# Kernel optimization log

Hardware: AMD Instinct MI355X
Metric: run time of the kernel (lower is better)

Reference implementation:

```python
import jax, jax.numpy as jnp
import numpy as np

V = 50257       # vocab size (leaves of Huffman tree)
N_DEC = V - 1   # internal decision nodes
D = 1024        # input_size
N_EX = 8192     # number of examples (tokens)
MAX_LEN = 24    # max Huffman path depth


def setup_inputs() -> dict:
    key = jax.random.key(0)
    k_x, k_w, k_t, k_p, k_c, k_l = jax.random.split(key, 6)
    x = jax.random.normal(k_x, (N_EX, D), dtype=jnp.float32)
    W = jax.random.normal(k_w, (N_DEC, D), dtype=jnp.float32) * 0.02
    t = jax.random.randint(k_t, (N_EX,), 0, V, dtype=jnp.int32)
    # padded per-leaf tree paths: decision-node indices and +/-1 branch codes
    paths = jax.random.randint(k_p, (V, MAX_LEN), 0, N_DEC, dtype=jnp.int32)
    codes = jnp.where(jax.random.bernoulli(k_c, 0.5, (V, MAX_LEN)), 1.0, -1.0).astype(jnp.float32)
    lens = jax.random.randint(k_l, (V,), 1, MAX_LEN + 1, dtype=jnp.int32)
    return {"x": x, "W": W, "t": t, "paths": paths, "codes": codes, "lens": lens}


def reference(x, W, t, paths, codes, lens):
    # Per-example tree path: gather the decision nodes / codes for each target leaf.
    node_idx = paths[t]            # [N_EX, MAX_LEN] int32
    code = codes[t]                # [N_EX, MAX_LEN] +/-1
    mask = (jnp.arange(MAX_LEN)[None, :] < lens[t][:, None]).astype(x.dtype)  # [N_EX, MAX_LEN]
    # Irregular gather of W rows along each path, then per-step dot products.
    Wp = W[node_idx]               # [N_EX, MAX_LEN, D]
    wxy = code * jnp.einsum('nd,nld->nl', x, Wp)   # [N_EX, MAX_LEN]
    # Per-decision binary log-loss: log(1 + exp(-wxy)), masked to true path length.
    ls = jax.nn.softplus(-wxy) * mask
    return ls.sum()
```

## Files before the change

### kernel.cpp

```cpp
#include <hip/hip_runtime.h>
#include <math.h>

#define HS_D       1024
#define HS_MAXLEN  24
#define HS_SPW     6

__global__ __launch_bounds__(256) void hsm_loss_kernel(
    const float* __restrict__ x,
    const float* __restrict__ W,
    const int*   __restrict__ t,
    const int*   __restrict__ paths,
    const float* __restrict__ codes,
    const int*   __restrict__ lens,
    float*       __restrict__ out)
{
    const int n    = blockIdx.x;
    const int tid  = threadIdx.x;
    const int wave = tid >> 6;
    const int lane = tid & 63;

    const int leaf = t[n];
    const int L    = lens[leaf];

    int   node[HS_SPW];
    float code[HS_SPW];
#pragma unroll
    for (int s = 0; s < HS_SPW; ++s) {
        const int l = wave + 4 * s;
        node[s] = paths[leaf * HS_MAXLEN + l];
        code[s] = codes[leaf * HS_MAXLEN + l];
    }

    const float4* x4 = (const float4*)(x + (size_t)n * HS_D);
    float4 xf[4];
#pragma unroll
    for (int j = 0; j < 4; ++j)
        xf[j] = x4[j * 64 + lane];

    float4 wf[HS_SPW][4];
#pragma unroll
    for (int s = 0; s < HS_SPW; ++s) {
        const float4* w4 = (const float4*)(W + (size_t)node[s] * HS_D);
#pragma unroll
        for (int j = 0; j < 4; ++j)
            wf[s][j] = w4[j * 64 + lane];
    }

    float dot[HS_SPW];
#pragma unroll
    for (int s = 0; s < HS_SPW; ++s) {
        float d = 0.0f;
#pragma unroll
        for (int j = 0; j < 4; ++j) {
            d += xf[j].x * wf[s][j].x + xf[j].y * wf[s][j].y
               + xf[j].z * wf[s][j].z + xf[j].w * wf[s][j].w;
        }
        dot[s] = d;
    }

#pragma unroll
    for (int off = 32; off > 0; off >>= 1) {
#pragma unroll
        for (int s = 0; s < HS_SPW; ++s)
            dot[s] += __shfl_down(dot[s], off);
    }

    float local = 0.0f;
    if (lane == 0) {
#pragma unroll
        for (int s = 0; s < HS_SPW; ++s) {
            const int l = wave + 4 * s;
            const float z = -code[s] * dot[s];
            const float sp = fmaxf(z, 0.0f) + log1pf(expf(-fabsf(z)));
            local += (l < L) ? sp : 0.0f;
        }
    }

    __shared__ float sred[4];
    if (lane == 0) sred[wave] = local;
    __syncthreads();
    if (tid == 0) {
        const float blocksum = sred[0] + sred[1] + sred[2] + sred[3];
        atomicAdd(out, blocksum);
    }
}

extern "C" void kernel_launch(void* const* d_in, const int* in_sizes, int n_in,
                              void* d_out, int out_size, void* d_ws, size_t ws_size,
                              hipStream_t stream) {
    const float* x     = (const float*)d_in[0];
    const float* W     = (const float*)d_in[1];
    const int*   t     = (const int*)  d_in[2];
    const int*   paths = (const int*)  d_in[3];
    const float* codes = (const float*)d_in[4];
    const int*   lens  = (const int*)  d_in[5];
    float* out = (float*)d_out;

    const int n_ex = in_sizes[2];

    hipMemsetAsync(out, 0, sizeof(float), stream);

    hsm_loss_kernel<<<n_ex, 256, 0, stream>>>(x, W, t, paths, codes, lens, out);
}
```

Before: 394.0 us.

## Assign one example per wave, loop only over valid path steps, bucket atomics

Each wavefront now handles a single example, broadcasts that example's path nodes and codes with lane shuffles, and walks only the first L steps in groups of four. Before, every step up to the maximum depth was loaded whether or not it was masked out. This removes the W row gathers for padded steps, which are on average about half of all steps. The single global atomic is replaced by atomics spread over 512 workspace buckets, summed by a small second kernel. The trade-offs are wave divergence from uneven path lengths, an extra kernel launch plus a larger memset, and possibly less memory-level parallelism per wave.

```diff
diff --git a/kernel.cpp b/kernel.cpp
--- a/kernel.cpp
+++ b/kernel.cpp
@@ -3,33 +3,23 @@
 
 #define HS_D       1024
 #define HS_MAXLEN  24
-#define HS_SPW     6
+#define HS_NBUCKET 512
 
-__global__ __launch_bounds__(256) void hsm_loss_kernel(
+__global__ __launch_bounds__(256, 4) void hsm_wave_kernel(
     const float* __restrict__ x,
     const float* __restrict__ W,
     const int*   __restrict__ t,
     const int*   __restrict__ paths,
     const float* __restrict__ codes,
     const int*   __restrict__ lens,
-    float*       __restrict__ out)
+    float*       __restrict__ ws)
 {
-    const int n    = blockIdx.x;
     const int tid  = threadIdx.x;
-    const int wave = tid >> 6;
     const int lane = tid & 63;
+    const int n    = blockIdx.x * 4 + (tid >> 6);
 
     const int leaf = t[n];
     const int L    = lens[leaf];
-
-    int   node[HS_SPW];
-    float code[HS_SPW];
-#pragma unroll
-    for (int s = 0; s < HS_SPW; ++s) {
-        const int l = wave + 4 * s;
-        node[s] = paths[leaf * HS_MAXLEN + l];
-        code[s] = codes[leaf * HS_MAXLEN + l];
-    }
 
     const float4* x4 = (const float4*)(x + (size_t)n * HS_D);
     float4 xf[4];
@@ -37,52 +27,80 @@
     for (int j = 0; j < 4; ++j)
         xf[j] = x4[j * 64 + lane];
 
-    float4 wf[HS_SPW][4];
-#pragma unroll
-    for (int s = 0; s < HS_SPW; ++s) {
-        const float4* w4 = (const float4*)(W + (size_t)node[s] * HS_D);
-#pragma unroll
-        for (int j = 0; j < 4; ++j)
-            wf[s][j] = w4[j * 64 + lane];
-    }
-
-    float dot[HS_SPW];
-#pragma unroll
-    for (int s = 0; s < HS_SPW; ++s) {
-        float d = 0.0f;
-#pragma unroll
-        for (int j = 0; j < 4; ++j) {
-            d += xf[j].x * wf[s][j].x + xf[j].y * wf[s][j].y
-               + xf[j].z * wf[s][j].z + xf[j].w * wf[s][j].w;
-        }
-        dot[s] = d;
-    }
-
-#pragma unroll
-    for (int off = 32; off > 0; off >>= 1) {
-#pragma unroll
-        for (int s = 0; s < HS_SPW; ++s)
-            dot[s] += __shfl_down(dot[s], off);
+    int   node_l = 0;
+    float code_l = 0.0f;
+    if (lane < HS_MAXLEN) {
+        node_l = paths[leaf * HS_MAXLEN + lane];
+        code_l = codes[leaf * HS_MAXLEN + lane];
     }
 
     float local = 0.0f;
-    if (lane == 0) {
+
+    for (int b = 0; b < L; b += 4) {
+        int   nd[4];
+        float cd[4];
 #pragma unroll
-        for (int s = 0; s < HS_SPW; ++s) {
-            const int l = wave + 4 * s;
-            const float z = -code[s] * dot[s];
-            const float sp = fmaxf(z, 0.0f) + log1pf(expf(-fabsf(z)));
-            local += (l < L) ? sp : 0.0f;
+        for (int s = 0; s < 4; ++s) {
+            const int  l = b + s;
+            const int  src = (l < L) ? l : 0;
+            nd[s] = __shfl(node_l, src);
+            cd[s] = __shfl(code_l, src);
+        }
+
+        float4 wf[4][4];
+#pragma unroll
+        for (int s = 0; s < 4; ++s) {
+            const float4* w4 = (const float4*)(W + (size_t)nd[s] * HS_D);
+#pragma unroll
+            for (int j = 0; j < 4; ++j)
+                wf[s][j] = w4[j * 64 + lane];
+        }
+
+        float dot[4];
+#pragma unroll
+        for (int s = 0; s < 4; ++s) {
+            float d = 0.0f;
+#pragma unroll
+            for (int j = 0; j < 4; ++j) {
+                d += xf[j].x * wf[s][j].x + xf[j].y * wf[s][j].y
+                   + xf[j].z * wf[s][j].z + xf[j].w * wf[s][j].w;
+            }
+            dot[s] = d;
+        }
+
+#pragma unroll
+        for (int off = 32; off > 0; off >>= 1) {
+#pragma unroll
+            for (int s = 0; s < 4; ++s)
+                dot[s] += __shfl_down(dot[s], off);
+        }
+
+        if (lane == 0) {
+#pragma unroll
+            for (int s = 0; s < 4; ++s) {
+                const float z  = -cd[s] * dot[s];
+                const float sp = fmaxf(z, 0.0f) + log1pf(expf(-fabsf(z)));
+                local += (b + s < L) ? sp : 0.0f;
+            }
         }
     }
 
-    __shared__ float sred[4];
-    if (lane == 0) sred[wave] = local;
-    __syncthreads();
-    if (tid == 0) {
-        const float blocksum = sred[0] + sred[1] + sred[2] + sred[3];
-        atomicAdd(out, blocksum);
-    }
+    if (lane == 0)
+        atomicAdd(&ws[n & (HS_NBUCKET - 1)], local);
+}
+
+__global__ __launch_bounds__(64) void hsm_finish_kernel(
+    const float* __restrict__ ws, float* __restrict__ out)
+{
+    const int lane = threadIdx.x;
+    float s = 0.0f;
+#pragma unroll
+    for (int k = 0; k < HS_NBUCKET / 64; ++k)
+        s += ws[lane + 64 * k];
+#pragma unroll
+    for (int off = 32; off > 0; off >>= 1)
+        s += __shfl_down(s, off);
+    if (lane == 0) out[0] = s;
 }
 
 extern "C" void kernel_launch(void* const* d_in, const int* in_sizes, int n_in,
@@ -95,10 +113,12 @@
     const float* codes = (const float*)d_in[4];
     const int*   lens  = (const int*)  d_in[5];
     float* out = (float*)d_out;
+    float* ws  = (float*)d_ws;
 
     const int n_ex = in_sizes[2];
 
-    hipMemsetAsync(out, 0, sizeof(float), stream);
+    hipMemsetAsync(ws, 0, HS_NBUCKET * sizeof(float), stream);
 
-    hsm_loss_kernel<<<n_ex, 256, 0, stream>>>(x, W, t, paths, codes, lens, out);
+    hsm_wave_kernel<<<n_ex / 4, 256, 0, stream>>>(x, W, t, paths, codes, lens, ws);
+    hsm_finish_kernel<<<1, 64, 0, stream>>>(ws, out);
 }
```

Result: faster. 335.5 us (-14.8%).
